# Optimization experiments

Hardware: AMD Instinct MI355X
Metric: run time of the kernel (lower is better)

Reference implementation:

```python
import jax, jax.numpy as jnp
import numpy as np

N_U, N_I, D_IN_U, D_IN_I, D, D_QOL, B = 4096, 4096, 256, 256, 256, 4, 8192

def _w(key, shape, scale=0.05):
    return (jax.random.normal(key, shape) * scale).astype(jnp.float32)

def setup_inputs() -> dict:
    key = jax.random.key(0)
    ks = jax.random.split(key, 24)
    inp = {
        "x_u": jax.random.normal(ks[0], (N_U, D_IN_U), jnp.float32),
        "x_i": jax.random.normal(ks[1], (N_I, D_IN_I), jnp.float32),
        "social_adj": jax.random.randint(ks[2], (N_U, N_U), 0, 2, jnp.int32),
        "ui_adj": jax.random.randint(ks[3], (N_U, N_I), 0, 2, jnp.int32),
        "user_idx": jax.random.randint(ks[4], (B,), 0, N_U, jnp.int32),
        "item_idx": jax.random.randint(ks[5], (B,), 0, N_I, jnp.int32),
        "q_u": jax.random.normal(ks[6], (N_U, D_QOL), jnp.float32),
        # params (Linear stored as [in, out]; y = x @ W + b)
        "user_W": _w(ks[7], (D_IN_U, D)), "user_b": jnp.zeros((D,), jnp.float32),
        "item_W": _w(ks[8], (D_IN_I, D)), "item_b": jnp.zeros((D,), jnp.float32),
        "soc_W": _w(ks[9], (D, D)), "soc_a": _w(ks[10], (2 * D,)),
        "cnt_W": _w(ks[11], (D, D)), "cnt_a": _w(ks[12], (2 * D,)),
        "gate_W": _w(ks[13], (D_QOL, D)), "gate_b": jnp.zeros((D,), jnp.float32),
        "qproj_W": _w(ks[14], (D_QOL, D)), "qproj_b": jnp.zeros((D,), jnp.float32),
        "alpha_q": jnp.float32(0.3),
        "pred_W1": _w(ks[15], (2 * D, D)), "pred_b1": jnp.zeros((D,), jnp.float32),
        "pred_W2": _w(ks[16], (D, 1)), "pred_b2": jnp.zeros((1,), jnp.float32),
    }
    return inp

def _gat(Wh_src, Wh_dst, a, adj):
    """GAT additive attention: src rows attend over dst cols where adj!=0.
    Rows with no neighbors produce zero output (matches nan_to_num + zeroing)."""
    d = Wh_src.shape[-1]
    a1 = Wh_src @ a[:d]          # [N_src]
    a2 = Wh_dst @ a[d:]          # [N_dst]
    e = jax.nn.leaky_relu(a1[:, None] + a2[None, :], 0.2)  # [N_src, N_dst]
    mask = adj != 0
    neg_inf = jnp.float32(-jnp.inf)
    m = jnp.max(jnp.where(mask, e, neg_inf), axis=-1, keepdims=True)
    m = jnp.where(jnp.isfinite(m), m, 0.0)  # guard empty rows
    ex = jnp.where(mask, jnp.exp(e - m), 0.0)
    denom = jnp.sum(ex, axis=-1, keepdims=True)
    alpha = jnp.where(denom > 0, ex / jnp.where(denom > 0, denom, 1.0), 0.0)
    out = alpha @ Wh_dst
    return out, alpha

def reference(x_u, x_i, social_adj, ui_adj, user_idx, item_idx, q_u,
              user_W, user_b, item_W, item_b, soc_W, soc_a, cnt_W, cnt_a,
              gate_W, gate_b, qproj_W, qproj_b, alpha_q,
              pred_W1, pred_b1, pred_W2, pred_b2):
    h_u = x_u @ user_W + user_b               # [N_u, D]
    h_i = x_i @ item_W + item_b               # [N_i, D]
    # social attention (users over users)
    Wh = h_u @ soc_W
    soc_msg, alpha_s = _gat(Wh, Wh, soc_a, social_adj)
    # content attention (users over items)
    Wu = h_u @ cnt_W
    Wi = h_i @ cnt_W
    cnt_msg, alpha_c = _gat(Wu, Wi, cnt_a, ui_adj)
    h_u_out = jax.nn.elu(soc_msg + cnt_msg + h_u)
    # QoL gate
    gate = jax.nn.sigmoid(q_u @ gate_W + gate_b)
    qproj = q_u @ qproj_W + qproj_b
    h_u_out = h_u_out + alpha_q * gate * qproj
    # pair prediction (dropout inactive at eval)
    cat = jnp.concatenate([h_u_out[user_idx], h_i[item_idx]], axis=-1)  # [B, 2D]
    hid = jax.nn.relu(cat @ pred_W1 + pred_b1)
    r = (hid @ pred_W2 + pred_b2)[..., 0]
    r_hat = 1.0 + 4.0 * jax.nn.sigmoid(r)
    return r_hat, alpha_s, alpha_c
```

## Files before the change

### kernel.cpp

```cpp
#include <hip/hip_runtime.h>

typedef unsigned short u16;
typedef unsigned int u32;
typedef unsigned char u8;
typedef unsigned long long u64;
typedef float f32x4 __attribute__((ext_vector_type(4)));
typedef __bf16 bf16x8 __attribute__((ext_vector_type(8)));

#define NU 4096
#define DD 256
#define BB 8192

__device__ inline u16 f2b(float f) {
    u32 u = __builtin_bit_cast(u32, f);
    u32 r = (u + 0x7fffu + ((u >> 16) & 1u)) >> 16;
    return (u16)r;
}
__device__ inline float lrelu(float x) { return x > 0.f ? x : 0.2f * x; }

#define BARRIER_LGKM() asm volatile("s_waitcnt lgkmcnt(0)\ns_barrier" ::: "memory")

__global__ __launch_bounds__(256) void k_pro(
    const float* __restrict__ x_u, const float* __restrict__ x_i,
    const float* __restrict__ user_W, const float* __restrict__ item_W, const float* __restrict__ pred_W1,
    const float* __restrict__ soc_W, const float* __restrict__ soc_a,
    const float* __restrict__ cnt_W, const float* __restrict__ cnt_a,
    const float* __restrict__ user_b, const float* __restrict__ item_b,
    u16* __restrict__ xu_b, u16* __restrict__ xi_b,
    u16* __restrict__ uWt, u16* __restrict__ iWt, u16* __restrict__ p1Wt,
    float* __restrict__ uvec,
    u16* __restrict__ WusT, u16* __restrict__ WicT,
    float* __restrict__ b_us, float* __restrict__ b_ic) {
    __shared__ float t[64][65];
    __shared__ float sa[256];
    const int b = blockIdx.x;
    const int tid = threadIdx.x;

    if (b < 1024) {
        const float* in = (b < 512) ? x_u : x_i;
        u16* out = (b < 512) ? xu_b : xi_b;
        int i = (b & 511) * 256 + tid;
        const float4 v0 = *(const float4*)(in + (size_t)i * 8);
        const float4 v1 = *(const float4*)(in + (size_t)i * 8 + 4);
        u16 u[8] = {f2b(v0.x), f2b(v0.y), f2b(v0.z), f2b(v0.w),
                    f2b(v1.x), f2b(v1.y), f2b(v1.z), f2b(v1.w)};
        *(uint4*)(out + (size_t)i * 8) = *(uint4*)u;
    } else if (b < 1088) {
        int j = b - 1024;
        const float* in;
        u16* out;
        int R;
        if (j < 16) { in = user_W; out = uWt; R = 256; }
        else if (j < 32) { in = item_W; out = iWt; R = 256; j -= 16; }
        else { in = pred_W1; out = p1Wt; R = 512; j -= 32; }
        int rb = (j >> 2) * 64, cb = (j & 3) * 64;
        for (int k = 0; k < 16; ++k) {
            int idx = k * 256 + tid;
            int lr = idx >> 6, lc = idx & 63;
            t[lr][lc] = in[(size_t)(rb + lr) * 256 + cb + lc];
        }
        __syncthreads();
        for (int k = 0; k < 16; ++k) {
            int idx = k * 256 + tid;
            int lr = idx >> 6, lc = idx & 63;
            out[(size_t)(cb + lr) * R + rb + lc] = f2b(t[lc][lr]);
        }
    } else if (b < 1092) {
        int bb = b - 1088;
        const float* W = (bb < 2) ? soc_W : cnt_W;
        const float* a = ((bb < 2) ? soc_a : cnt_a) + (bb & 1) * 256;
        int lane = tid & 63, wv = tid >> 6;
        sa[tid] = a[tid];
        __syncthreads();
        for (int rr = 0; rr < 64; ++rr) {
            int in = wv * 64 + rr;
            float4 w4 = *(const float4*)(W + (size_t)in * 256 + lane * 4);
            float acc = w4.x * sa[lane * 4] + w4.y * sa[lane * 4 + 1] + w4.z * sa[lane * 4 + 2] + w4.w * sa[lane * 4 + 3];
#pragma unroll
            for (int off = 32; off; off >>= 1) acc += __shfl_down(acc, off);
            if (lane == 0) uvec[bb * 256 + in] = acc;
        }
    } else {
        int j = b - 1092;
        int p = j >> 4;
        int tile = j & 15;
        const float* A = p ? item_W : user_W;
        const float* Bw = p ? cnt_W : soc_W;
        const float* bvec = p ? item_b : user_b;
        u16* outT = p ? WicT : WusT;
        float* outb = p ? b_ic : b_us;
        int m0 = (tile >> 2) * 64, n0 = (tile & 3) * 64;
        int m = m0 + (tid >> 4) * 4, n = n0 + (tid & 15) * 4;
        float acc[4][4];
#pragma unroll
        for (int i = 0; i < 4; ++i)
#pragma unroll
            for (int k = 0; k < 4; ++k) acc[i][k] = 0.f;
        for (int k0 = 0; k0 < 256; k0 += 4) {
            float aa[4][4], bb2[4][4];
#pragma unroll
            for (int i = 0; i < 4; ++i) {
                float4 v = *(const float4*)(A + (size_t)(m + i) * 256 + k0);
                aa[i][0] = v.x; aa[i][1] = v.y; aa[i][2] = v.z; aa[i][3] = v.w;
            }
#pragma unroll
            for (int k = 0; k < 4; ++k) {
                float4 v = *(const float4*)(Bw + (size_t)(k0 + k) * 256 + n);
                bb2[k][0] = v.x; bb2[k][1] = v.y; bb2[k][2] = v.z; bb2[k][3] = v.w;
            }
#pragma unroll
            for (int i = 0; i < 4; ++i)
#pragma unroll
                for (int k = 0; k < 4; ++k)
#pragma unroll
                    for (int jj = 0; jj < 4; ++jj) acc[i][jj] += aa[i][k] * bb2[k][jj];
        }
#pragma unroll
        for (int i = 0; i < 4; ++i)
#pragma unroll
            for (int jj = 0; jj < 4; ++jj) outT[(size_t)(n + jj) * 256 + m + i] = f2b(acc[i][jj]);
        if (tile >> 2 == 0 && tid < 64) {
            int nn = n0 + tid;
            float s = 0.f;
            for (int k = 0; k < 256; ++k) s += bvec[k] * Bw[(size_t)k * 256 + nn];
            outb[nn] = s;
        }
    }
}

__global__ __launch_bounds__(256) void k_gemm4(
    const u16* __restrict__ xu_b, const u16* __restrict__ xi_b,
    const u16* __restrict__ uWt, const u16* __restrict__ iWt,
    const u16* __restrict__ WusT, const u16* __restrict__ WicT,
    const float* __restrict__ user_b, const float* __restrict__ item_b,
    const float* __restrict__ b_us, const float* __restrict__ b_ic,
    float* __restrict__ h_u_f, float* __restrict__ h_i_f, u16* __restrict__ h_i_b,
    u16* __restrict__ WhT, u16* __restrict__ WiT) {
    const int z = blockIdx.z;
    const int M = 4096, N = 256, K = 256;
    const u16* A = (z == 0 || z == 2) ? xu_b : xi_b;
    const u16* Bt = (z == 0) ? uWt : (z == 1) ? iWt : (z == 2) ? WusT : WicT;
    const float* bias = (z == 0) ? user_b : (z == 1) ? item_b : (z == 2) ? b_us : b_ic;
    float* Cf = (z == 0) ? h_u_f : (z == 1) ? h_i_f : nullptr;
    u16* Cb = (z == 1) ? h_i_b : nullptr;
    u16* Cbt = (z == 2) ? WhT : (z == 3) ? WiT : nullptr;

    __shared__ u16 As[64 * 64];
    __shared__ u16 Bs[64 * 64];
    const int tid = threadIdx.x;
    const int lane = tid & 63, wv = tid >> 6;
    const int bm = blockIdx.x * 64, bn = blockIdx.y * 64;
    const int wm = (wv >> 1) * 32, wn = (wv & 1) * 32;
    f32x4 acc[2][2];
#pragma unroll
    for (int i = 0; i < 2; i++)
#pragma unroll
        for (int j = 0; j < 2; j++) acc[i][j] = f32x4{0.f, 0.f, 0.f, 0.f};

    char* Ab = (char*)As;
    char* Bb = (char*)Bs;
    const int r = tid >> 2;
    const int ib0 = (tid & 3) * 32;
    const int swz = (r & 7) << 4;

    for (int k0 = 0; k0 < K; k0 += 64) {
        const uint4* ga = (const uint4*)(A + (size_t)(bm + r) * K + k0 + (ib0 >> 1));
        const uint4* gb = (const uint4*)(Bt + (size_t)(bn + r) * K + k0 + (ib0 >> 1));
        uint4 va0 = ga[0], va1 = ga[1];
        uint4 vb0 = gb[0], vb1 = gb[1];
        __syncthreads();
        *(uint4*)(Ab + r * 128 + ((ib0) ^ swz)) = va0;
        *(uint4*)(Ab + r * 128 + ((ib0 + 16) ^ swz)) = va1;
        *(uint4*)(Bb + r * 128 + ((ib0) ^ swz)) = vb0;
        *(uint4*)(Bb + r * 128 + ((ib0 + 16) ^ swz)) = vb1;
        __syncthreads();
#pragma unroll
        for (int kh = 0; kh < 2; ++kh) {
            bf16x8 af[2], bfr[2];
#pragma unroll
            for (int mf = 0; mf < 2; ++mf) {
                int row = wm + mf * 16 + (lane & 15);
                int kb = kh * 64 + ((lane >> 4) << 4);
                af[mf] = *(const bf16x8*)(Ab + row * 128 + (kb ^ ((row & 7) << 4)));
            }
#pragma unroll
            for (int nf = 0; nf < 2; ++nf) {
                int row = wn + nf * 16 + (lane & 15);
                int kb = kh * 64 + ((lane >> 4) << 4);
                bfr[nf] = *(const bf16x8*)(Bb + row * 128 + (kb ^ ((row & 7) << 4)));
            }
#pragma unroll
            for (int mf = 0; mf < 2; ++mf)
#pragma unroll
                for (int nf = 0; nf < 2; ++nf)
                    acc[mf][nf] = __builtin_amdgcn_mfma_f32_16x16x32_bf16(af[mf], bfr[nf], acc[mf][nf], 0, 0, 0);
        }
    }
#pragma unroll
    for (int mf = 0; mf < 2; ++mf) {
#pragma unroll
        for (int nf = 0; nf < 2; ++nf) {
            int col = bn + wn + nf * 16 + (lane & 15);
            int row0 = bm + wm + mf * 16 + ((lane >> 4) << 2);
            float bv = bias[col];
            float v[4];
#pragma unroll
            for (int q = 0; q < 4; ++q) {
                float x = acc[mf][nf][q] + bv;
                v[q] = x;
                if (Cf) Cf[(size_t)(row0 + q) * N + col] = x;
                if (Cb) Cb[(size_t)(row0 + q) * N + col] = f2b(x);
            }
            if (Cbt) {
                uint2 p;
                p.x = (u32)f2b(v[0]) | ((u32)f2b(v[1]) << 16);
                p.y = (u32)f2b(v[2]) | ((u32)f2b(v[3]) << 16);
                *(uint2*)(Cbt + (size_t)col * M + row0) = p;
            }
        }
    }
}

__global__ __launch_bounds__(256) void k_gemv_a(const float* __restrict__ h_u, const float* __restrict__ h_i,
                                                const float* __restrict__ uvec, float* __restrict__ avec) {
    int tid = threadIdx.x, lane = tid & 63, wv = tid >> 6;
    int ib = blockIdx.x * 64;
    const float* H = (wv == 3) ? h_i : h_u;
    const float* u = uvec + wv * 256;
    float4 u4 = *(const float4*)(u + lane * 4);
    for (int rr = 0; rr < 64; ++rr) {
        int row = ib + rr;
        float4 h4 = *(const float4*)(H + (size_t)row * 256 + lane * 4);
        float acc = h4.x * u4.x + h4.y * u4.y + h4.z * u4.z + h4.w * u4.w;
#pragma unroll
        for (int off = 32; off; off >>= 1) acc += __shfl_down(acc, off);
        if (lane == 0) avec[wv * 4096 + row] = acc;
    }
}

__global__ __launch_bounds__(256) void k_maxfinal(const float* __restrict__ avec, float* __restrict__ Mh) {
    __shared__ float red[256];
    int t = threadIdx.x;
    for (int z = 0; z < 2; ++z) {
        const float* a2 = avec + z * 8192 + 4096;
        float m = -1e30f;
        for (int i = t; i < 4096; i += 256) m = fmaxf(m, a2[i]);
        red[t] = m;
        __syncthreads();
        for (int s = 128; s; s >>= 1) {
            if (t < s) red[t] = fmaxf(red[t], red[t + s]);
            __syncthreads();
        }
        if (t == 0) Mh[z] = red[0];
        __syncthreads();
    }
}

__global__ __launch_bounds__(256) void k_scan(const int* __restrict__ adjS, const int* __restrict__ adjC,
                                              const float* __restrict__ avec, const float* __restrict__ Mh,
                                              float* __restrict__ dpart, u8* __restrict__ bits) {
    int z = blockIdx.z;
    const int* adj = z ? adjC : adjS;
    const float* a1 = avec + z * 8192;
    const float* a2 = a1 + 4096;
    u8* bz = bits + (size_t)z * 2097152;
    float mhg = Mh[z];
    int ib = blockIdx.x * 64, jb = blockIdx.y * 512;
    int lane = threadIdx.x & 63, wv = threadIdx.x >> 6;
    float4 A0 = *(const float4*)(a2 + jb + lane * 8);
    float4 A1 = *(const float4*)(a2 + jb + lane * 8 + 4);
    for (int rr = 0; rr < 16; ++rr) {
        int row = ib + wv * 16 + rr;
        float a1r = a1[row];
        float mr = lrelu(a1r + mhg);
        const int4* p = (const int4*)(adj + (size_t)row * 4096 + jb + lane * 8);
        int4 v0 = p[0], v1 = p[1];
        u32 b = (u32)(v0.x != 0) | ((u32)(v0.y != 0) << 1) | ((u32)(v0.z != 0) << 2) | ((u32)(v0.w != 0) << 3) |
                ((u32)(v1.x != 0) << 4) | ((u32)(v1.y != 0) << 5) | ((u32)(v1.z != 0) << 6) | ((u32)(v1.w != 0) << 7);
        bz[(size_t)row * 512 + (jb >> 3) + lane] = (u8)b;
        float acc = 0.f;
        acc += v0.x ? __expf(lrelu(a1r + A0.x) - mr) : 0.f;
        acc += v0.y ? __expf(lrelu(a1r + A0.y) - mr) : 0.f;
        acc += v0.z ? __expf(lrelu(a1r + A0.z) - mr) : 0.f;
        acc += v0.w ? __expf(lrelu(a1r + A0.w) - mr) : 0.f;
        acc += v1.x ? __expf(lrelu(a1r + A1.x) - mr) : 0.f;
        acc += v1.y ? __expf(lrelu(a1r + A1.y) - mr) : 0.f;
        acc += v1.z ? __expf(lrelu(a1r + A1.z) - mr) : 0.f;
        acc += v1.w ? __expf(lrelu(a1r + A1.w) - mr) : 0.f;
#pragma unroll
        for (int off = 32; off; off >>= 1) acc += __shfl_down(acc, off);
        if (lane == 0) dpart[((size_t)z * 8 + blockIdx.y) * 4096 + row] = acc;
    }
}

__global__ __launch_bounds__(256) void k_dreduce(const float* __restrict__ dpart, float* __restrict__ invd) {
    int i = blockIdx.x * 256 + threadIdx.x;
    if (i < 8192) {
        int z = i >> 12, r = i & 4095;
        float d = 0.f;
#pragma unroll
        for (int s = 0; s < 8; ++s) d += dpart[((size_t)z * 8 + s) * 4096 + r];
        invd[i] = d > 0.f ? 1.f / d : 0.f;
    }
}

__global__ __launch_bounds__(512, 4) void k_flash(const u8* __restrict__ bits,
                                                  const float* __restrict__ avec, const float* __restrict__ Mh,
                                                  const float* __restrict__ invd,
                                                  const u16* __restrict__ WhT, const u16* __restrict__ WiT,
                                                  float* __restrict__ out, float* __restrict__ msgpart) {
    const int z = blockIdx.z;
    const int ib = blockIdx.x * 64;
    const int jb = blockIdx.y * 1024;
    const int tid = threadIdx.x, lane = tid & 63, wv = tid >> 6;
    const u8* bz = bits + (size_t)z * 2097152;
    const float* a1 = avec + z * 8192;
    const float* a2 = a1 + 4096;
    const u16* Pt = z ? WiT : WhT;
    float* alpha = out + 8192 + (size_t)z * 16777216;
    const float mhg = Mh[z];
    const float* inv = invd + z * 4096;

    __shared__ float a2s[1024];
    __shared__ u16 Atile[2 * 64 * 64];
    __shared__ float s_a1[64], s_mr[64], s_inv[64];
    char* Ab = (char*)Atile;

    const int row = wv * 8 + (lane >> 3);
    const int cg = lane & 7;
    const int gr = ib + row;
    const int bbase = jb >> 3;

    {
        float2 v = *(const float2*)(a2 + jb + tid * 2);
        *(float2*)(a2s + tid * 2) = v;
        if (tid < 64) {
            float a = a1[ib + tid];
            s_a1[tid] = a;
            s_mr[tid] = lrelu(a + mhg);
            s_inv[tid] = inv[ib + tid];
        }
    }
    __syncthreads();

    f32x4 acc[4][2];
#pragma unroll
    for (int i = 0; i < 4; i++)
#pragma unroll
        for (int j = 0; j < 2; j++) acc[i][j] = f32x4{0.f, 0.f, 0.f, 0.f};

    float4 stA, stB;
    const float a1r = s_a1[row], mr = s_mr[row], ivr = s_inv[row];
    const int wswz = (row & 7) << 4;

    auto compute_tile = [&](int js, int buf) {
        const int j0 = js * 64;
        u32 byte = bz[(size_t)gr * 512 + bbase + js * 8 + cg];
        const float4 a2a = *(const float4*)(a2s + j0 + cg * 8);
        const float4 a2b = *(const float4*)(a2s + j0 + cg * 8 + 4);
        float av[8] = {a2a.x, a2a.y, a2a.z, a2a.w, a2b.x, a2b.y, a2b.z, a2b.w};
        float al[8];
#pragma unroll
        for (int k = 0; k < 8; ++k) {
            float e = lrelu(a1r + av[k]) - mr;
            float x = ((byte >> k) & 1) ? __expf(e) : 0.f;
            al[k] = x * ivr;
        }
        stA = float4{al[0], al[1], al[2], al[3]};
        stB = float4{al[4], al[5], al[6], al[7]};
        u16 pk[8];
#pragma unroll
        for (int k = 0; k < 8; ++k) pk[k] = f2b(al[k]);
        *(uint4*)(Ab + buf * 8192 + row * 128 + ((cg * 16) ^ wswz)) = *(uint4*)pk;
    };

    compute_tile(0, 0);
    BARRIER_LGKM();

    for (int js = 0; js < 16; ++js) {
        const int j0 = js * 64;
        const int buf = js & 1;
        float* ap = alpha + (size_t)gr * 4096 + jb + j0 + cg * 8;
        *(float4*)ap = stA;
        *(float4*)(ap + 4) = stB;
#pragma unroll
        for (int kh = 0; kh < 2; ++kh) {
            bf16x8 bfr[2];
#pragma unroll
            for (int nf = 0; nf < 2; ++nf) {
                int n = wv * 32 + nf * 16 + (lane & 15);
                bfr[nf] = *(const bf16x8*)(Pt + (size_t)n * 4096 + jb + j0 + kh * 32 + ((lane >> 4) << 3));
            }
#pragma unroll
            for (int mf = 0; mf < 4; ++mf) {
                int row_a = mf * 16 + (lane & 15);
                int kb = kh * 64 + ((lane >> 4) << 4);
                bf16x8 af = *(const bf16x8*)(Ab + buf * 8192 + row_a * 128 + (kb ^ ((row_a & 7) << 4)));
#pragma unroll
                for (int nf = 0; nf < 2; ++nf)
                    acc[mf][nf] = __builtin_amdgcn_mfma_f32_16x16x32_bf16(af, bfr[nf], acc[mf][nf], 0, 0, 0);
            }
        }
        if (js < 15) compute_tile(js + 1, buf ^ 1);
        BARRIER_LGKM();
    }

    float* mp = msgpart + ((size_t)(z * 4 + blockIdx.y) * 4096 + ib) * 256;
#pragma unroll
    for (int mf = 0; mf < 4; ++mf) {
        int r0 = mf * 16 + ((lane >> 4) << 2);
#pragma unroll
        for (int nf = 0; nf < 2; ++nf) {
            int col = wv * 32 + nf * 16 + (lane & 15);
#pragma unroll
            for (int q = 0; q < 4; ++q) mp[(size_t)(r0 + q) * 256 + col] = acc[mf][nf][q];
        }
    }
}

__global__ __launch_bounds__(256) void k_post(const float* __restrict__ msgpart, const float* __restrict__ h_u,
                                              const float* __restrict__ q_u,
                                              const float* __restrict__ gate_W, const float* __restrict__ gate_b,
                                              const float* __restrict__ qproj_W, const float* __restrict__ qproj_b,
                                              const float* __restrict__ alpha_q, u16* __restrict__ huo_b) {
    int i = blockIdx.x;
    int n = threadIdx.x;
    float s = 0.f;
#pragma unroll
    for (int p = 0; p < 8; ++p) s += msgpart[((size_t)p * 4096 + i) * 256 + n];
    float v = s + h_u[(size_t)i * 256 + n];
    v = v > 0.f ? v : expm1f(v);
    float q0 = q_u[i * 4 + 0], q1 = q_u[i * 4 + 1], q2 = q_u[i * 4 + 2], q3 = q_u[i * 4 + 3];
    float g = q0 * gate_W[n] + q1 * gate_W[256 + n] + q2 * gate_W[512 + n] + q3 * gate_W[768 + n] + gate_b[n];
    g = 1.f / (1.f + __expf(-g));
    float qp = q0 * qproj_W[n] + q1 * qproj_W[256 + n] + q2 * qproj_W[512 + n] + q3 * qproj_W[768 + n] + qproj_b[n];
    float o = v + alpha_q[0] * g * qp;
    huo_b[(size_t)i * 256 + n] = f2b(o);
}

__global__ __launch_bounds__(512) void k_pred(const u16* __restrict__ huo_b, const u16* __restrict__ h_i_b,
                                              const int* __restrict__ uidx, const int* __restrict__ iidx,
                                              const u16* __restrict__ Bt, const float* __restrict__ b1,
                                              const float* __restrict__ W2, const float* __restrict__ b2,
                                              float* __restrict__ out) {
    __shared__ u16 As[64 * 512];
    __shared__ float redL[512];
    const int tid = threadIdx.x, lane = tid & 63, wv = tid >> 6;
    const int bm = blockIdx.x * 64;
    char* Ab = (char*)As;

    {
        const int r = tid >> 3;
        const int uix = uidx[bm + r], iix = iidx[bm + r];
        const int sswz = (r & 7) << 4;
#pragma unroll
        for (int c = 0; c < 8; ++c) {
            int e = c * 64 + (tid & 7) * 8;
            const u16* src = (e < 256) ? (huo_b + (size_t)uix * 256 + e) : (h_i_b + (size_t)iix * 256 + (e - 256));
            uint4 v = *(const uint4*)src;
            *(uint4*)(Ab + r * 1024 + ((e * 2) ^ sswz)) = v;
        }
    }
    __syncthreads();

    const int n0 = wv * 32;
    f32x4 acc[4][2];
#pragma unroll
    for (int i = 0; i < 4; i++)
#pragma unroll
        for (int j = 0; j < 2; j++) acc[i][j] = f32x4{0.f, 0.f, 0.f, 0.f};

    for (int ks = 0; ks < 16; ++ks) {
        bf16x8 bfr[2];
#pragma unroll
        for (int nf = 0; nf < 2; ++nf)
            bfr[nf] = *(const bf16x8*)(Bt + (size_t)(n0 + nf * 16 + (lane & 15)) * 512 + ks * 32 + ((lane >> 4) << 3));
#pragma unroll
        for (int mf = 0; mf < 4; ++mf) {
            int ra = mf * 16 + (lane & 15);
            bf16x8 af = *(const bf16x8*)(Ab + ra * 1024 + ((ks * 64 + ((lane >> 4) << 4)) ^ ((ra & 7) << 4)));
#pragma unroll
            for (int nf = 0; nf < 2; ++nf)
                acc[mf][nf] = __builtin_amdgcn_mfma_f32_16x16x32_bf16(af, bfr[nf], acc[mf][nf], 0, 0, 0);
        }
    }

    float b1v[2], w2v[2];
#pragma unroll
    for (int nf = 0; nf < 2; ++nf) {
        int col = n0 + nf * 16 + (lane & 15);
        b1v[nf] = b1[col];
        w2v[nf] = W2[col];
    }
#pragma unroll
    for (int mf = 0; mf < 4; ++mf) {
#pragma unroll
        for (int q = 0; q < 4; ++q) {
            float val = 0.f;
#pragma unroll
            for (int nf = 0; nf < 2; ++nf) val += fmaxf(acc[mf][nf][q] + b1v[nf], 0.f) * w2v[nf];
#pragma unroll
            for (int off = 1; off < 16; off <<= 1) val += __shfl_xor(val, off);
            if ((lane & 15) == 0) redL[wv * 64 + mf * 16 + ((lane >> 4) << 2) + q] = val;
        }
    }
    __syncthreads();
    if (tid < 64) {
        float r = b2[0];
#pragma unroll
        for (int w = 0; w < 8; ++w) r += redL[w * 64 + tid];
        out[bm + tid] = 1.f + 4.f / (1.f + __expf(-r));
    }
}

extern "C" void kernel_launch(void* const* d_in, const int* in_sizes, int n_in,
                              void* d_out, int out_size, void* d_ws, size_t ws_size,
                              hipStream_t stream) {
    const float* x_u = (const float*)d_in[0];
    const float* x_i = (const float*)d_in[1];
    const int* adjS = (const int*)d_in[2];
    const int* adjC = (const int*)d_in[3];
    const int* uidx = (const int*)d_in[4];
    const int* iidx = (const int*)d_in[5];
    const float* q_u = (const float*)d_in[6];
    const float* user_W = (const float*)d_in[7];
    const float* user_b = (const float*)d_in[8];
    const float* item_W = (const float*)d_in[9];
    const float* item_b = (const float*)d_in[10];
    const float* soc_W = (const float*)d_in[11];
    const float* soc_a = (const float*)d_in[12];
    const float* cnt_W = (const float*)d_in[13];
    const float* cnt_a = (const float*)d_in[14];
    const float* gate_W = (const float*)d_in[15];
    const float* gate_b = (const float*)d_in[16];
    const float* qproj_W = (const float*)d_in[17];
    const float* qproj_b = (const float*)d_in[18];
    const float* alpha_q = (const float*)d_in[19];
    const float* pred_W1 = (const float*)d_in[20];
    const float* pred_b1 = (const float*)d_in[21];
    const float* pred_W2 = (const float*)d_in[22];
    const float* pred_b2 = (const float*)d_in[23];
    float* out = (float*)d_out;

    char* w = (char*)d_ws;
    size_t off = 0;
    auto alloc = [&](size_t bytes) -> void* {
        void* p = w + off;
        off = (off + bytes + 255) & ~(size_t)255;
        return p;
    };
    u16* xu_b = (u16*)alloc((size_t)NU * DD * 2);
    u16* xi_b = (u16*)alloc((size_t)NU * DD * 2);
    u16* uWt = (u16*)alloc(256 * 256 * 2);
    u16* iWt = (u16*)alloc(256 * 256 * 2);
    u16* p1Wt = (u16*)alloc(512 * 256 * 2);
    u16* WusT = (u16*)alloc(256 * 256 * 2);
    u16* WicT = (u16*)alloc(256 * 256 * 2);
    float* b_us = (float*)alloc(256 * 4);
    float* b_ic = (float*)alloc(256 * 4);
    float* uvec = (float*)alloc(4 * 256 * 4);
    float* h_u_f = (float*)alloc((size_t)NU * DD * 4);
    float* h_i_f = (float*)alloc((size_t)NU * DD * 4);
    u16* h_i_b = (u16*)alloc((size_t)NU * DD * 2);
    u16* WhT = (u16*)alloc((size_t)NU * DD * 2);
    u16* WiT = (u16*)alloc((size_t)NU * DD * 2);
    float* avec = (float*)alloc(4 * 4096 * 4);
    float* Mh = (float*)alloc(2 * 4);
    float* dpart = (float*)alloc((size_t)2 * 8 * 4096 * 4);
    float* invd = (float*)alloc((size_t)2 * 4096 * 4);
    u8* bits = (u8*)alloc((size_t)2 * 2097152);
    float* msgpart = (float*)alloc((size_t)2 * 4 * 4096 * 256 * 4);
    u16* huo_b = (u16*)alloc((size_t)NU * DD * 2);
    (void)in_sizes; (void)n_in; (void)out_size; (void)ws_size;

    k_pro<<<1124, 256, 0, stream>>>(x_u, x_i, user_W, item_W, pred_W1, soc_W, soc_a, cnt_W, cnt_a,
                                    user_b, item_b, xu_b, xi_b, uWt, iWt, p1Wt, uvec, WusT, WicT, b_us, b_ic);
    k_gemm4<<<dim3(64, 4, 4), 256, 0, stream>>>(xu_b, xi_b, uWt, iWt, WusT, WicT, user_b, item_b, b_us, b_ic,
                                                h_u_f, h_i_f, h_i_b, WhT, WiT);
    k_gemv_a<<<64, 256, 0, stream>>>(h_u_f, h_i_f, uvec, avec);
    k_maxfinal<<<1, 256, 0, stream>>>(avec, Mh);
    k_scan<<<dim3(64, 8, 2), 256, 0, stream>>>(adjS, adjC, avec, Mh, dpart, bits);
    k_dreduce<<<32, 256, 0, stream>>>(dpart, invd);
    k_flash<<<dim3(64, 4, 2), 512, 0, stream>>>(bits, avec, Mh, invd, WhT, WiT, out, msgpart);
    k_post<<<4096, 256, 0, stream>>>(msgpart, h_u_f, q_u, gate_W, gate_b, qproj_W, qproj_b, alpha_q, huo_b);
    k_pred<<<128, 512, 0, stream>>>(huo_b, h_i_b, uidx, iidx, p1Wt, pred_b1, pred_W2, pred_b2, out);
}
```

Baseline: 202.9 us.

## Fuse max and denominator reductions, split flash wider, prefetch B fragments, bf16 partials

Drops k_maxfinal by folding the column max into k_gemv_a with an order-preserving encoded atomicMax, and drops k_dreduce by having k_flash sum the denominator partials itself. Doubles k_flash's column split (512 columns per block, 1024 blocks) and stores the adjacency bitmask in a layout that lets each thread read one u64 of bits up front. Global B-operand fragments are now register double-buffered one step ahead. Message partials are stored as bf16 to halve their traffic, at some precision cost, and k_post now sums 16 partials instead of 8.

```diff
diff --git a/kernel.cpp b/kernel.cpp
--- a/kernel.cpp
+++ b/kernel.cpp
@@ -16,7 +16,11 @@
     u32 r = (u + 0x7fffu + ((u >> 16) & 1u)) >> 16;
     return (u16)r;
 }
+__device__ inline float b2f(u16 v) { return __builtin_bit_cast(float, (u32)v << 16); }
 __device__ inline float lrelu(float x) { return x > 0.f ? x : 0.2f * x; }
+__device__ inline float decmax(u32 e) {
+    return __builtin_bit_cast(float, (e >> 31) ? (e & 0x7fffffffu) : ~e);
+}
 
 #define BARRIER_LGKM() asm volatile("s_waitcnt lgkmcnt(0)\ns_barrier" ::: "memory")
 
@@ -30,7 +34,7 @@
     u16* __restrict__ uWt, u16* __restrict__ iWt, u16* __restrict__ p1Wt,
     float* __restrict__ uvec,
     u16* __restrict__ WusT, u16* __restrict__ WicT,
-    float* __restrict__ b_us, float* __restrict__ b_ic) {
+    float* __restrict__ b_us, float* __restrict__ b_ic, u32* __restrict__ MhEnc) {
     __shared__ float t[64][65];
     __shared__ float sa[256];
     const int b = blockIdx.x;
@@ -67,6 +71,7 @@
         }
     } else if (b < 1092) {
         int bb = b - 1088;
+        if (bb == 0 && tid < 2) MhEnc[tid] = 0u;
         const float* W = (bb < 2) ? soc_W : cnt_W;
         const float* a = ((bb < 2) ? soc_a : cnt_a) + (bb & 1) * 256;
         int lane = tid & 63, wv = tid >> 6;
@@ -222,53 +227,46 @@
 }
 
 __global__ __launch_bounds__(256) void k_gemv_a(const float* __restrict__ h_u, const float* __restrict__ h_i,
-                                                const float* __restrict__ uvec, float* __restrict__ avec) {
+                                                const float* __restrict__ uvec, float* __restrict__ avec,
+                                                u32* __restrict__ MhEnc) {
     int tid = threadIdx.x, lane = tid & 63, wv = tid >> 6;
     int ib = blockIdx.x * 64;
     const float* H = (wv == 3) ? h_i : h_u;
     const float* u = uvec + wv * 256;
     float4 u4 = *(const float4*)(u + lane * 4);
+    float runm = -1e30f;
     for (int rr = 0; rr < 64; ++rr) {
         int row = ib + rr;
         float4 h4 = *(const float4*)(H + (size_t)row * 256 + lane * 4);
         float acc = h4.x * u4.x + h4.y * u4.y + h4.z * u4.z + h4.w * u4.w;
 #pragma unroll
         for (int off = 32; off; off >>= 1) acc += __shfl_down(acc, off);
-        if (lane == 0) avec[wv * 4096 + row] = acc;
-    }
-}
-
-__global__ __launch_bounds__(256) void k_maxfinal(const float* __restrict__ avec, float* __restrict__ Mh) {
-    __shared__ float red[256];
-    int t = threadIdx.x;
-    for (int z = 0; z < 2; ++z) {
-        const float* a2 = avec + z * 8192 + 4096;
-        float m = -1e30f;
-        for (int i = t; i < 4096; i += 256) m = fmaxf(m, a2[i]);
-        red[t] = m;
-        __syncthreads();
-        for (int s = 128; s; s >>= 1) {
-            if (t < s) red[t] = fmaxf(red[t], red[t + s]);
-            __syncthreads();
-        }
-        if (t == 0) Mh[z] = red[0];
-        __syncthreads();
+        if (lane == 0) {
+            avec[wv * 4096 + row] = acc;
+            runm = fmaxf(runm, acc);
+        }
+    }
+    if (lane == 0 && (wv & 1)) {
+        u32 b = __builtin_bit_cast(u32, runm);
+        u32 e = (b >> 31) ? ~b : (b | 0x80000000u);
+        atomicMax(&MhEnc[wv >> 1], e);
     }
 }
 
 __global__ __launch_bounds__(256) void k_scan(const int* __restrict__ adjS, const int* __restrict__ adjC,
-                                              const float* __restrict__ avec, const float* __restrict__ Mh,
+                                              const float* __restrict__ avec, const u32* __restrict__ MhEnc,
                                               float* __restrict__ dpart, u8* __restrict__ bits) {
     int z = blockIdx.z;
     const int* adj = z ? adjC : adjS;
     const float* a1 = avec + z * 8192;
     const float* a2 = a1 + 4096;
     u8* bz = bits + (size_t)z * 2097152;
-    float mhg = Mh[z];
+    float mhg = decmax(MhEnc[z]);
     int ib = blockIdx.x * 64, jb = blockIdx.y * 512;
     int lane = threadIdx.x & 63, wv = threadIdx.x >> 6;
     float4 A0 = *(const float4*)(a2 + jb + lane * 8);
     float4 A1 = *(const float4*)(a2 + jb + lane * 8 + 4);
+    const int boff = blockIdx.y * 64 + (lane & 7) * 8 + (lane >> 3);
     for (int rr = 0; rr < 16; ++rr) {
         int row = ib + wv * 16 + rr;
         float a1r = a1[row];
@@ -277,7 +275,7 @@
         int4 v0 = p[0], v1 = p[1];
         u32 b = (u32)(v0.x != 0) | ((u32)(v0.y != 0) << 1) | ((u32)(v0.z != 0) << 2) | ((u32)(v0.w != 0) << 3) |
                 ((u32)(v1.x != 0) << 4) | ((u32)(v1.y != 0) << 5) | ((u32)(v1.z != 0) << 6) | ((u32)(v1.w != 0) << 7);
-        bz[(size_t)row * 512 + (jb >> 3) + lane] = (u8)b;
+        bz[(size_t)row * 512 + boff] = (u8)b;
         float acc = 0.f;
         acc += v0.x ? __expf(lrelu(a1r + A0.x) - mr) : 0.f;
         acc += v0.y ? __expf(lrelu(a1r + A0.y) - mr) : 0.f;
@@ -293,119 +291,122 @@
     }
 }
 
-__global__ __launch_bounds__(256) void k_dreduce(const float* __restrict__ dpart, float* __restrict__ invd) {
-    int i = blockIdx.x * 256 + threadIdx.x;
-    if (i < 8192) {
-        int z = i >> 12, r = i & 4095;
-        float d = 0.f;
-#pragma unroll
-        for (int s = 0; s < 8; ++s) d += dpart[((size_t)z * 8 + s) * 4096 + r];
-        invd[i] = d > 0.f ? 1.f / d : 0.f;
-    }
-}
-
 __global__ __launch_bounds__(512, 4) void k_flash(const u8* __restrict__ bits,
-                                                  const float* __restrict__ avec, const float* __restrict__ Mh,
-                                                  const float* __restrict__ invd,
+                                                  const float* __restrict__ avec, const u32* __restrict__ MhEnc,
+                                                  const float* __restrict__ dpart,
                                                   const u16* __restrict__ WhT, const u16* __restrict__ WiT,
-                                                  float* __restrict__ out, float* __restrict__ msgpart) {
+                                                  float* __restrict__ out, u16* __restrict__ msgpart) {
     const int z = blockIdx.z;
     const int ib = blockIdx.x * 64;
-    const int jb = blockIdx.y * 1024;
+    const int jb = blockIdx.y * 512;
     const int tid = threadIdx.x, lane = tid & 63, wv = tid >> 6;
     const u8* bz = bits + (size_t)z * 2097152;
     const float* a1 = avec + z * 8192;
     const float* a2 = a1 + 4096;
     const u16* Pt = z ? WiT : WhT;
     float* alpha = out + 8192 + (size_t)z * 16777216;
-    const float mhg = Mh[z];
-    const float* inv = invd + z * 4096;
-
-    __shared__ float a2s[1024];
+
+    __shared__ float a2s[512];
     __shared__ u16 Atile[2 * 64 * 64];
     __shared__ float s_a1[64], s_mr[64], s_inv[64];
     char* Ab = (char*)Atile;
 
+    a2s[tid] = a2[jb + tid];
+    if (tid < 64) {
+        float a = a1[ib + tid];
+        float mhg = decmax(MhEnc[z]);
+        s_a1[tid] = a;
+        s_mr[tid] = lrelu(a + mhg);
+        float d = 0.f;
+#pragma unroll
+        for (int s = 0; s < 8; ++s) d += dpart[((size_t)(z * 8 + s)) * 4096 + ib + tid];
+        s_inv[tid] = d > 0.f ? 1.f / d : 0.f;
+    }
+    __syncthreads();
+
     const int row = wv * 8 + (lane >> 3);
     const int cg = lane & 7;
     const int gr = ib + row;
-    const int bbase = jb >> 3;
-
-    {
-        float2 v = *(const float2*)(a2 + jb + tid * 2);
-        *(float2*)(a2s + tid * 2) = v;
-        if (tid < 64) {
-            float a = a1[ib + tid];
-            s_a1[tid] = a;
-            s_mr[tid] = lrelu(a + mhg);
-            s_inv[tid] = inv[ib + tid];
-        }
-    }
-    __syncthreads();
-
-    f32x4 acc[4][2];
-#pragma unroll
-    for (int i = 0; i < 4; i++)
-#pragma unroll
-        for (int j = 0; j < 2; j++) acc[i][j] = f32x4{0.f, 0.f, 0.f, 0.f};
-
-    float4 stA, stB;
+    const u64 b64 = *(const u64*)(bz + (size_t)gr * 512 + (jb >> 9) * 64 + cg * 8);
     const float a1r = s_a1[row], mr = s_mr[row], ivr = s_inv[row];
     const int wswz = (row & 7) << 4;
 
-    auto compute_tile = [&](int js, int buf) {
-        const int j0 = js * 64;
-        u32 byte = bz[(size_t)gr * 512 + bbase + js * 8 + cg];
-        const float4 a2a = *(const float4*)(a2s + j0 + cg * 8);
-        const float4 a2b = *(const float4*)(a2s + j0 + cg * 8 + 4);
+    const u16* ptb0 = Pt + (size_t)(wv * 32 + (lane & 15)) * 4096 + jb + ((lane >> 4) << 3);
+    const u16* ptb1 = ptb0 + (size_t)16 * 4096;
+
+    f32x4 acc[4][2];
+#pragma unroll
+    for (int i = 0; i < 4; i++)
+#pragma unroll
+        for (int j = 0; j < 2; j++) acc[i][j] = f32x4{0.f, 0.f, 0.f, 0.f};
+
+    float al[8];
+    auto compute_al = [&](int js, int buf) {
+        const float4 a2a = *(const float4*)(a2s + js * 64 + cg * 8);
+        const float4 a2b = *(const float4*)(a2s + js * 64 + cg * 8 + 4);
+        u32 byte = (u32)(b64 >> (js * 8)) & 0xffu;
         float av[8] = {a2a.x, a2a.y, a2a.z, a2a.w, a2b.x, a2b.y, a2b.z, a2b.w};
-        float al[8];
 #pragma unroll
         for (int k = 0; k < 8; ++k) {
             float e = lrelu(a1r + av[k]) - mr;
-            float x = ((byte >> k) & 1) ? __expf(e) : 0.f;
-            al[k] = x * ivr;
-        }
-        stA = float4{al[0], al[1], al[2], al[3]};
-        stB = float4{al[4], al[5], al[6], al[7]};
+            al[k] = ((byte >> k) & 1) ? __expf(e) * ivr : 0.f;
+        }
         u16 pk[8];
 #pragma unroll
         for (int k = 0; k < 8; ++k) pk[k] = f2b(al[k]);
         *(uint4*)(Ab + buf * 8192 + row * 128 + ((cg * 16) ^ wswz)) = *(uint4*)pk;
     };
 
-    compute_tile(0, 0);
+    compute_al(0, 0);
     BARRIER_LGKM();
 
-    for (int js = 0; js < 16; ++js) {
-        const int j0 = js * 64;
+    bf16x8 bcur[2][2], bnxt[2][2];
+#pragma unroll
+    for (int kh = 0; kh < 2; ++kh) {
+        bcur[kh][0] = *(const bf16x8*)(ptb0 + kh * 32);
+        bcur[kh][1] = *(const bf16x8*)(ptb1 + kh * 32);
+    }
+
+    for (int js = 0; js < 8; ++js) {
         const int buf = js & 1;
-        float* ap = alpha + (size_t)gr * 4096 + jb + j0 + cg * 8;
-        *(float4*)ap = stA;
-        *(float4*)(ap + 4) = stB;
+        {
+            float4 sA = {al[0], al[1], al[2], al[3]};
+            float4 sB = {al[4], al[5], al[6], al[7]};
+            float* ap = alpha + (size_t)gr * 4096 + jb + js * 64 + cg * 8;
+            *(float4*)ap = sA;
+            *(float4*)(ap + 4) = sB;
+        }
+        if (js < 7) {
+#pragma unroll
+            for (int kh = 0; kh < 2; ++kh) {
+                bnxt[kh][0] = *(const bf16x8*)(ptb0 + (js + 1) * 64 + kh * 32);
+                bnxt[kh][1] = *(const bf16x8*)(ptb1 + (js + 1) * 64 + kh * 32);
+            }
+        }
 #pragma unroll
         for (int kh = 0; kh < 2; ++kh) {
-            bf16x8 bfr[2];
-#pragma unroll
-            for (int nf = 0; nf < 2; ++nf) {
-                int n = wv * 32 + nf * 16 + (lane & 15);
-                bfr[nf] = *(const bf16x8*)(Pt + (size_t)n * 4096 + jb + j0 + kh * 32 + ((lane >> 4) << 3));
-            }
 #pragma unroll
             for (int mf = 0; mf < 4; ++mf) {
-                int row_a = mf * 16 + (lane & 15);
+                int ra = mf * 16 + (lane & 15);
                 int kb = kh * 64 + ((lane >> 4) << 4);
-                bf16x8 af = *(const bf16x8*)(Ab + buf * 8192 + row_a * 128 + (kb ^ ((row_a & 7) << 4)));
+                bf16x8 af = *(const bf16x8*)(Ab + buf * 8192 + ra * 128 + (kb ^ ((ra & 7) << 4)));
 #pragma unroll
                 for (int nf = 0; nf < 2; ++nf)
-                    acc[mf][nf] = __builtin_amdgcn_mfma_f32_16x16x32_bf16(af, bfr[nf], acc[mf][nf], 0, 0, 0);
-            }
-        }
-        if (js < 15) compute_tile(js + 1, buf ^ 1);
+                    acc[mf][nf] = __builtin_amdgcn_mfma_f32_16x16x32_bf16(af, bcur[kh][nf], acc[mf][nf], 0, 0, 0);
+            }
+        }
+        if (js < 7) compute_al(js + 1, buf ^ 1);
         BARRIER_LGKM();
-    }
-
-    float* mp = msgpart + ((size_t)(z * 4 + blockIdx.y) * 4096 + ib) * 256;
+        if (js < 7) {
+#pragma unroll
+            for (int kh = 0; kh < 2; ++kh) {
+                bcur[kh][0] = bnxt[kh][0];
+                bcur[kh][1] = bnxt[kh][1];
+            }
+        }
+    }
+
+    u16* mp = msgpart + ((size_t)(z * 8 + blockIdx.y) * 4096 + ib) * 256;
 #pragma unroll
     for (int mf = 0; mf < 4; ++mf) {
         int r0 = mf * 16 + ((lane >> 4) << 2);
@@ -413,12 +414,12 @@
         for (int nf = 0; nf < 2; ++nf) {
             int col = wv * 32 + nf * 16 + (lane & 15);
 #pragma unroll
-            for (int q = 0; q < 4; ++q) mp[(size_t)(r0 + q) * 256 + col] = acc[mf][nf][q];
-        }
-    }
-}
-
-__global__ __launch_bounds__(256) void k_post(const float* __restrict__ msgpart, const float* __restrict__ h_u,
+            for (int q = 0; q < 4; ++q) mp[(size_t)(r0 + q) * 256 + col] = f2b(acc[mf][nf][q]);
+        }
+    }
+}
+
+__global__ __launch_bounds__(256) void k_post(const u16* __restrict__ msgpart, const float* __restrict__ h_u,
                                               const float* __restrict__ q_u,
                                               const float* __restrict__ gate_W, const float* __restrict__ gate_b,
                                               const float* __restrict__ qproj_W, const float* __restrict__ qproj_b,
@@ -427,7 +428,7 @@
     int n = threadIdx.x;
     float s = 0.f;
 #pragma unroll
-    for (int p = 0; p < 8; ++p) s += msgpart[((size_t)p * 4096 + i) * 256 + n];
+    for (int p = 0; p < 16; ++p) s += b2f(msgpart[((size_t)p * 4096 + i) * 256 + n]);
     float v = s + h_u[(size_t)i * 256 + n];
     v = v > 0.f ? v : expm1f(v);
     float q0 = q_u[i * 4 + 0], q1 = q_u[i * 4 + 1], q2 = q_u[i * 4 + 2], q3 = q_u[i * 4 + 3];
@@ -565,23 +566,21 @@
     u16* WhT = (u16*)alloc((size_t)NU * DD * 2);
     u16* WiT = (u16*)alloc((size_t)NU * DD * 2);
     float* avec = (float*)alloc(4 * 4096 * 4);
-    float* Mh = (float*)alloc(2 * 4);
+    u32* MhEnc = (u32*)alloc(2 * 4);
     float* dpart = (float*)alloc((size_t)2 * 8 * 4096 * 4);
-    float* invd = (float*)alloc((size_t)2 * 4096 * 4);
     u8* bits = (u8*)alloc((size_t)2 * 2097152);
-    float* msgpart = (float*)alloc((size_t)2 * 4 * 4096 * 256 * 4);
+    u16* msgpart = (u16*)alloc((size_t)16 * 4096 * 256 * 2);
     u16* huo_b = (u16*)alloc((size_t)NU * DD * 2);
     (void)in_sizes; (void)n_in; (void)out_size; (void)ws_size;
 
     k_pro<<<1124, 256, 0, stream>>>(x_u, x_i, user_W, item_W, pred_W1, soc_W, soc_a, cnt_W, cnt_a,
-                                    user_b, item_b, xu_b, xi_b, uWt, iWt, p1Wt, uvec, WusT, WicT, b_us, b_ic);
+                                    user_b, item_b, xu_b, xi_b, uWt, iWt, p1Wt, uvec, WusT, WicT,
+                                    b_us, b_ic, MhEnc);
     k_gemm4<<<dim3(64, 4, 4), 256, 0, stream>>>(xu_b, xi_b, uWt, iWt, WusT, WicT, user_b, item_b, b_us, b_ic,
                                                 h_u_f, h_i_f, h_i_b, WhT, WiT);
-    k_gemv_a<<<64, 256, 0, stream>>>(h_u_f, h_i_f, uvec, avec);
-    k_maxfinal<<<1, 256, 0, stream>>>(avec, Mh);
-    k_scan<<<dim3(64, 8, 2), 256, 0, stream>>>(adjS, adjC, avec, Mh, dpart, bits);
-    k_dreduce<<<32, 256, 0, stream>>>(dpart, invd);
-    k_flash<<<dim3(64, 4, 2), 512, 0, stream>>>(bits, avec, Mh, invd, WhT, WiT, out, msgpart);
+    k_gemv_a<<<64, 256, 0, stream>>>(h_u_f, h_i_f, uvec, avec, MhEnc);
+    k_scan<<<dim3(64, 8, 2), 256, 0, stream>>>(adjS, adjC, avec, MhEnc, dpart, bits);
+    k_flash<<<dim3(64, 8, 2), 512, 0, stream>>>(bits, avec, MhEnc, dpart, WhT, WiT, out, msgpart);
     k_post<<<4096, 256, 0, stream>>>(msgpart, h_u_f, q_u, gate_W, gate_b, qproj_W, qproj_b, alpha_q, huo_b);
     k_pred<<<128, 512, 0, stream>>>(huo_b, h_i_b, uidx, iidx, p1Wt, pred_b1, pred_W2, pred_b2, out);
 }
```

Result: faster. 189.6 us (-6.6%).
